# Performance work log

Hardware: AMD Instinct MI355X
Metric: run time of the kernel (lower is better)

Reference implementation:

```python
import jax, jax.numpy as jnp
import numpy as np
import math

D = 1024      # d_model
H = 4096      # expert hidden
E = 8         # num_experts
K = 2         # top_k
CAP_FACTOR = 1.25
B, S = 4, 2048
T = B * S
CAP = int(math.ceil(CAP_FACTOR * T * K / E))  # 2560


def setup_inputs() -> dict:
    key = jax.random.key(0)
    ks = jax.random.split(key, 6)
    x  = jax.random.normal(ks[0], (B, S, D), dtype=jnp.float32)
    Wr = jax.random.normal(ks[1], (D, E), dtype=jnp.float32) * (1.0 / np.sqrt(D))
    W1 = jax.random.normal(ks[2], (E, D, H), dtype=jnp.float32) * (1.0 / np.sqrt(D))
    b1 = jnp.zeros((E, H), dtype=jnp.float32)
    W2 = jax.random.normal(ks[3], (E, H, D), dtype=jnp.float32) * (1.0 / np.sqrt(H))
    b2 = jnp.zeros((E, D), dtype=jnp.float32)
    return {"x": x, "Wr": Wr, "W1": W1, "b1": b1, "W2": W2, "b2": b2}


def reference(x, Wr, W1, b1, W2, b2):
    x_flat = x.reshape(T, D)

    # ---- Router: top-k softmax gating (temp = 1.0), renormalized weights ----
    logits = jnp.einsum('td,de->te', x_flat, Wr)
    probs = jax.nn.softmax(logits, axis=-1)
    topk_w, topk_idx = jax.lax.top_k(probs, K)            # [T,K]
    topk_w = topk_w / jnp.sum(topk_w, axis=-1, keepdims=True)

    # ---- Vectorized capacity-based dispatch ----
    e = topk_idx.reshape(-1)                               # [T*K] expert id per pair
    onehot = jax.nn.one_hot(e, E, dtype=jnp.int32)         # [T*K, E]
    pos_all = jnp.cumsum(onehot, axis=0) - 1               # slot within expert
    pos = jnp.take_along_axis(pos_all, e[:, None], axis=1)[:, 0]
    keep = pos < CAP
    # dropped pairs go to a dummy slot E*CAP (sliced off / zero-padded)
    dest = jnp.where(keep, e * CAP + pos, E * CAP)         # [T*K]

    x_pairs = jnp.repeat(x_flat, K, axis=0)                # [T*K, D]
    buf = jnp.zeros((E * CAP + 1, D), dtype=x.dtype).at[dest].set(x_pairs)
    expert_in = buf[:E * CAP].reshape(E, CAP, D)

    # ---- Grouped expert MLP (GELU) ----
    h = jax.nn.gelu(jnp.einsum('ecd,edh->ech', expert_in, W1) + b1[:, None, :])
    expert_out = jnp.einsum('ech,ehd->ecd', h, W2) + b2[:, None, :]

    # ---- Combine: gather back and weight; dropped tokens get zeros ----
    out_pad = jnp.concatenate(
        [expert_out.reshape(E * CAP, D), jnp.zeros((1, D), dtype=x.dtype)], axis=0)
    y_pairs = out_pad[dest] * topk_w.reshape(-1)[:, None]  # [T*K, D]
    y_flat = y_pairs.reshape(T, K, D).sum(axis=1)
    return y_flat.reshape(B, S, D)
```

## Files before the change

kernel.cpp:

```cpp
#include <hip/hip_runtime.h>
#include <stdint.h>

#define D_MODEL 1024
#define H_DIM   4096
#define NE      8
#define NCAP    2560
#define NTOK    8192
#define NPAIR   (NTOK * 2)

typedef __attribute__((ext_vector_type(8))) __bf16 bf16x8;
typedef __attribute__((ext_vector_type(4))) float  f32x4;
typedef __attribute__((ext_vector_type(8))) unsigned short ushort8;

__device__ __forceinline__ unsigned short f2bf(float f) {
  union { float f; unsigned u; } v; v.f = f;
  unsigned r = v.u + 0x7fffu + ((v.u >> 16) & 1u);
  return (unsigned short)(r >> 16);
}
__device__ __forceinline__ float bf2f(unsigned short s) {
  union { unsigned u; float f; } v; v.u = ((unsigned)s) << 16;
  return v.f;
}
__device__ __forceinline__ float gelu_tanh(float x) {
  float u = 0.7978845608028654f * (x + 0.044715f * x * x * x);
  float e = __expf(2.0f * u);
  float th = 1.0f - 2.0f / (e + 1.0f);
  return 0.5f * x * (1.0f + th);
}
__device__ __forceinline__ void load_lds16(const void* g, void* l) {
  __builtin_amdgcn_global_load_lds(
      (const __attribute__((address_space(1))) unsigned int*)g,
      (__attribute__((address_space(3))) unsigned int*)l, 16, 0, 0);
}

__global__ __launch_bounds__(256) void router_kernel(
    const float* __restrict__ x, const float* __restrict__ Wr,
    int* __restrict__ pair_e, float* __restrict__ pair_w) {
  int lane = threadIdx.x & 63;
  int t = blockIdx.x * 4 + (threadIdx.x >> 6);
  float acc[NE];
#pragma unroll
  for (int e = 0; e < NE; ++e) acc[e] = 0.0f;
  const float* xr = x + (size_t)t * D_MODEL;
  for (int d = lane; d < D_MODEL; d += 64) {
    float xv = xr[d];
#pragma unroll
    for (int e = 0; e < NE; ++e) acc[e] = fmaf(xv, Wr[d * NE + e], acc[e]);
  }
#pragma unroll
  for (int off = 32; off > 0; off >>= 1) {
#pragma unroll
    for (int e = 0; e < NE; ++e) acc[e] += __shfl_down(acc[e], off, 64);
  }
  if (lane == 0) {
    int i1 = 0;
#pragma unroll
    for (int e = 1; e < NE; ++e) if (acc[e] > acc[i1]) i1 = e;
    int i2 = (i1 == 0) ? 1 : 0;
#pragma unroll
    for (int e = 0; e < NE; ++e) if (e != i1 && acc[e] > acc[i2]) i2 = e;
    float p2 = expf(acc[i2] - acc[i1]);
    float inv = 1.0f / (1.0f + p2);
    pair_e[t * 2]     = i1;  pair_e[t * 2 + 1] = i2;
    pair_w[t * 2]     = inv;
    pair_w[t * 2 + 1] = p2 * inv;
  }
}

__global__ void assign_kernel(const int* __restrict__ pair_e,
                              int* __restrict__ pair_dest,
                              int* __restrict__ counts) {
  int lane = threadIdx.x;
  int run[NE];
#pragma unroll
  for (int e = 0; e < NE; ++e) run[e] = 0;
  unsigned long long below = (lane == 63) ? 0x7fffffffffffffffull
                                          : ((1ull << lane) - 1ull);
  for (int base = 0; base < NPAIR; base += 64) {
    int i = base + lane;
    int e = pair_e[i];
    int pos = 0;
#pragma unroll
    for (int ex = 0; ex < NE; ++ex) {
      unsigned long long m = __ballot(e == ex);
      if (e == ex) pos = run[ex] + __popcll(m & below);
      run[ex] += __popcll(m);
    }
    bool keep = pos < NCAP;
    pair_dest[i] = keep ? (e * NCAP + pos) : (NE * NCAP);
  }
  if (lane == 0) {
#pragma unroll
    for (int e = 0; e < NE; ++e) counts[e] = run[e] < NCAP ? run[e] : NCAP;
  }
}

__global__ __launch_bounds__(64) void dispatch_kernel(
    const float* __restrict__ x, const int* __restrict__ pair_dest,
    unsigned short* __restrict__ Xd) {
  int i = blockIdx.x;
  int dest = pair_dest[i];
  if (dest >= NE * NCAP) return;
  int lane = threadIdx.x;
  int t = i >> 1;
  const float4* xr = (const float4*)(x + (size_t)t * D_MODEL);
  ushort4* dr = (ushort4*)(Xd + (size_t)dest * D_MODEL);
#pragma unroll
  for (int c = 0; c < 4; ++c) {
    float4 v = xr[lane + c * 64];
    ushort4 o;
    o.x = f2bf(v.x); o.y = f2bf(v.y); o.z = f2bf(v.z); o.w = f2bf(v.w);
    dr[lane + c * 64] = o;
  }
}

__global__ __launch_bounds__(256) void transpose_cvt(
    const float* __restrict__ src, unsigned short* __restrict__ dst,
    int R, int C) {
  __shared__ float tile[64][65];
  int e = blockIdx.z;
  int c0 = blockIdx.x * 64, r0 = blockIdx.y * 64;
  int col = threadIdx.x & 63, rr = threadIdx.x >> 6;
  const float* s = src + (size_t)e * R * C;
#pragma unroll
  for (int it = 0; it < 16; ++it) {
    int row = it * 4 + rr;
    tile[row][col] = s[(size_t)(r0 + row) * C + c0 + col];
  }
  __syncthreads();
  unsigned short* d = dst + (size_t)e * R * C;
#pragma unroll
  for (int it = 0; it < 16; ++it) {
    int crow = it * 4 + rr;
    d[(size_t)(c0 + crow) * R + r0 + col] = f2bf(tile[col][crow]);
  }
}

__global__ __launch_bounds__(256, 2) void moe_gemm(
    const unsigned short* __restrict__ Abase,
    const unsigned short* __restrict__ Bbase,
    const float* __restrict__ bias,
    unsigned short* __restrict__ Cout,
    const int* __restrict__ counts,
    int M, int N, int K, int NBM, int do_gelu) {
  __shared__ char smem[65536];
  const int e = blockIdx.z;
  int r = blockIdx.x;
  int grp = r >> 4, lid = r & 15;
  int mg = NBM >> 2;
  int gm = grp % mg, gn = grp / mg;
  const int m0 = (gm * 4 + (lid & 3)) * 128;
  const int n0 = (gn * 4 + (lid >> 2)) * 128;
  const int cnt = counts[e];
  if (m0 >= cnt) return;

  const int tid = threadIdx.x;
  const int lane = tid & 63;
  const int wid = tid >> 6;
  const int wm = (wid & 1) * 64;
  const int wn = (wid >> 1) * 64;

  const unsigned short* A = Abase + (size_t)e * M * K;
  const unsigned short* B = Bbase + (size_t)e * N * K;

  f32x4 acc[4][4];
  f32x4 zero = {0.f, 0.f, 0.f, 0.f};
#pragma unroll
  for (int i = 0; i < 4; ++i)
#pragma unroll
    for (int j = 0; j < 4; ++j) acc[i][j] = zero;

  char* As0 = smem;
  char* Bs0 = smem + 16384;
  char* As1 = smem + 32768;
  char* Bs1 = smem + 49152;

  const unsigned short* ga[4];
  const unsigned short* gb[4];
  int ldso[4];
#pragma unroll
  for (int c = 0; c < 4; ++c) {
    int ci = c * 256 + wid * 64 + lane;
    int srow = ci >> 3;
    int sgc = (ci & 7) ^ (srow & 7);
    ga[c] = A + (size_t)(m0 + srow) * K + sgc * 8;
    gb[c] = B + (size_t)(n0 + srow) * K + sgc * 8;
    ldso[c] = (c * 256 + wid * 64) * 16;
  }

  auto stage = [&](char* As, char* Bs) {
#pragma unroll
    for (int c = 0; c < 4; ++c) {
      load_lds16(ga[c], As + ldso[c]);
      ga[c] += 64;
      load_lds16(gb[c], Bs + ldso[c]);
      gb[c] += 64;
    }
  };
  auto compute = [&](char* As, char* Bs) {
#pragma unroll
    for (int kk = 0; kk < 2; ++kk) {
      bf16x8 af[4], bfr[4];
      int lc = kk * 4 + (lane >> 4);
#pragma unroll
      for (int f = 0; f < 4; ++f) {
        int ar = wm + f * 16 + (lane & 15);
        af[f] = *(const bf16x8*)(As + ar * 128 + ((lc ^ (ar & 7)) * 16));
        int br = wn + f * 16 + (lane & 15);
        bfr[f] = *(const bf16x8*)(Bs + br * 128 + ((lc ^ (br & 7)) * 16));
      }
#pragma unroll
      for (int i = 0; i < 4; ++i)
#pragma unroll
        for (int j = 0; j < 4; ++j)
          acc[i][j] = __builtin_amdgcn_mfma_f32_16x16x32_bf16(
              af[i], bfr[j], acc[i][j], 0, 0, 0);
    }
  };

  const int KT = K >> 6;
  stage(As0, Bs0);
  for (int kt = 0; kt < KT; kt += 2) {
    __syncthreads();
    if (kt + 1 < KT) stage(As1, Bs1);
    compute(As0, Bs0);
    __syncthreads();
    if (kt + 2 < KT) stage(As0, Bs0);
    compute(As1, Bs1);
  }

  const float* be = bias + (size_t)e * N;
#pragma unroll
  for (int i = 0; i < 4; ++i) {
    int rbase = wm + i * 16 + (lane >> 4) * 4;
#pragma unroll
    for (int j = 0; j < 4; ++j) {
      int col = wn + j * 16 + (lane & 15);
      float bv = be[n0 + col];
#pragma unroll
      for (int r2 = 0; r2 < 4; ++r2) {
        float xv = acc[i][j][r2] + bv;
        if (do_gelu) xv = gelu_tanh(xv);
        *(unsigned short*)(smem + (rbase + r2) * 256 + col * 2) = f2bf(xv);
      }
    }
  }
  __syncthreads();
  const int r16 = tid >> 4, c16 = tid & 15;
#pragma unroll
  for (int it = 0; it < 8; ++it) {
    int row = it * 16 + r16;
    ushort8 v = *(const ushort8*)(smem + row * 256 + c16 * 16);
    *(ushort8*)(Cout + ((size_t)e * M + m0 + row) * N + n0 + c16 * 8) = v;
  }
}

__global__ __launch_bounds__(256) void combine_kernel(
    const unsigned short* __restrict__ Ebuf,
    const int* __restrict__ pair_dest,
    const float* __restrict__ pair_w,
    float* __restrict__ out) {
  int t = blockIdx.x;
  int d0 = threadIdx.x * 4;
  float4 r = {0.f, 0.f, 0.f, 0.f};
#pragma unroll
  for (int k = 0; k < 2; ++k) {
    int dest = pair_dest[t * 2 + k];
    if (dest < NE * NCAP) {
      float w = pair_w[t * 2 + k];
      ushort4 v = *(const ushort4*)(Ebuf + (size_t)dest * D_MODEL + d0);
      r.x += w * bf2f(v.x); r.y += w * bf2f(v.y);
      r.z += w * bf2f(v.z); r.w += w * bf2f(v.w);
    }
  }
  *(float4*)(out + (size_t)t * D_MODEL + d0) = r;
}

extern "C" void kernel_launch(void* const* d_in, const int* in_sizes, int n_in,
                              void* d_out, int out_size, void* d_ws, size_t ws_size,
                              hipStream_t stream) {
  const float* x  = (const float*)d_in[0];
  const float* Wr = (const float*)d_in[1];
  const float* W1 = (const float*)d_in[2];
  const float* b1 = (const float*)d_in[3];
  const float* W2 = (const float*)d_in[4];
  const float* b2 = (const float*)d_in[5];
  float* out = (float*)d_out;

  char* ws = (char*)d_ws;
  unsigned short* W1T  = (unsigned short*)(ws + 0);
  unsigned short* W2T  = (unsigned short*)(ws + 67108864);
  unsigned short* Xd   = (unsigned short*)(ws + 134217728);
  unsigned short* Ebuf = Xd;
  unsigned short* Hbuf = (unsigned short*)(ws + 176160768);
  int*   pair_e    = (int*)(ws + 343932928);
  float* pair_w    = (float*)(ws + 343998464);
  int*   pair_dest = (int*)(ws + 344064000);
  int*   counts    = (int*)(ws + 344129536);

  transpose_cvt<<<dim3(H_DIM / 64, D_MODEL / 64, NE), 256, 0, stream>>>(W1, W1T, D_MODEL, H_DIM);
  transpose_cvt<<<dim3(D_MODEL / 64, H_DIM / 64, NE), 256, 0, stream>>>(W2, W2T, H_DIM, D_MODEL);

  router_kernel<<<NTOK / 4, 256, 0, stream>>>(x, Wr, pair_e, pair_w);
  assign_kernel<<<1, 64, 0, stream>>>(pair_e, pair_dest, counts);
  dispatch_kernel<<<NPAIR, 64, 0, stream>>>(x, pair_dest, Xd);

  moe_gemm<<<dim3((NCAP / 128) * (H_DIM / 128), 1, NE), 256, 0, stream>>>(
      Xd, W1T, b1, Hbuf, counts, NCAP, H_DIM, D_MODEL, NCAP / 128, 1);
  moe_gemm<<<dim3((NCAP / 128) * (D_MODEL / 128), 1, NE), 256, 0, stream>>>(
      Hbuf, W2T, b2, Ebuf, counts, NCAP, D_MODEL, H_DIM, NCAP / 128, 0);

  combine_kernel<<<NTOK, 256, 0, stream>>>(Ebuf, pair_dest, pair_w, out);
}
```

Before: 890.5 us.

## Parallelize capacity assignment scan and single-buffer GEMM LDS for higher occupancy

The serial single-wave assign kernel is replaced by a 1024-thread block in which each thread counts 16 pairs, followed by wave shuffle prefix sums and a cross-wave scan in LDS. This targets the long serial loop over all pairs. Separately, the expert GEMM drops LDS double buffering to 32KB and raises launch bounds to 4 blocks per CU, relying on occupancy rather than in-block prefetch to hide global-to-LDS latency. This adds two syncs per K step and loses the overlap of loads with compute.

New measurement: 770.1 us. 1.16x faster.

```diff
diff --git a/kernel.cpp b/kernel.cpp
--- a/kernel.cpp
+++ b/kernel.cpp
@@ -67,31 +67,63 @@
   }
 }
 
-__global__ void assign_kernel(const int* __restrict__ pair_e,
-                              int* __restrict__ pair_dest,
-                              int* __restrict__ counts) {
-  int lane = threadIdx.x;
-  int run[NE];
-#pragma unroll
-  for (int e = 0; e < NE; ++e) run[e] = 0;
-  unsigned long long below = (lane == 63) ? 0x7fffffffffffffffull
-                                          : ((1ull << lane) - 1ull);
-  for (int base = 0; base < NPAIR; base += 64) {
-    int i = base + lane;
-    int e = pair_e[i];
-    int pos = 0;
-#pragma unroll
-    for (int ex = 0; ex < NE; ++ex) {
-      unsigned long long m = __ballot(e == ex);
-      if (e == ex) pos = run[ex] + __popcll(m & below);
-      run[ex] += __popcll(m);
-    }
-    bool keep = pos < NCAP;
-    pair_dest[i] = keep ? (e * NCAP + pos) : (NE * NCAP);
-  }
-  if (lane == 0) {
-#pragma unroll
-    for (int e = 0; e < NE; ++e) counts[e] = run[e] < NCAP ? run[e] : NCAP;
+__global__ __launch_bounds__(1024) void assign_kernel(
+    const int* __restrict__ pair_e, int* __restrict__ pair_dest,
+    int* __restrict__ counts) {
+  __shared__ int wtot[16][NE];
+  const int tid = threadIdx.x;
+  const int lane = tid & 63, w = tid >> 6;
+
+  int ids[16];
+  const int4* pe = (const int4*)(pair_e + tid * 16);
+#pragma unroll
+  for (int q = 0; q < 4; ++q) {
+    int4 v = pe[q];
+    ids[q * 4 + 0] = v.x; ids[q * 4 + 1] = v.y;
+    ids[q * 4 + 2] = v.z; ids[q * 4 + 3] = v.w;
+  }
+  int c[NE];
+#pragma unroll
+  for (int e = 0; e < NE; ++e) c[e] = 0;
+#pragma unroll
+  for (int j = 0; j < 16; ++j) c[ids[j]]++;
+
+  int incl[NE];
+#pragma unroll
+  for (int e = 0; e < NE; ++e) incl[e] = c[e];
+#pragma unroll
+  for (int d = 1; d < 64; d <<= 1) {
+#pragma unroll
+    for (int e = 0; e < NE; ++e) {
+      int u = __shfl_up(incl[e], d, 64);
+      if (lane >= d) incl[e] += u;
+    }
+  }
+  if (lane == 63) {
+#pragma unroll
+    for (int e = 0; e < NE; ++e) wtot[w][e] = incl[e];
+  }
+  __syncthreads();
+  if (tid < NE) {
+    int run = 0;
+#pragma unroll
+    for (int ww = 0; ww < 16; ++ww) {
+      int t2 = wtot[ww][tid];
+      wtot[ww][tid] = run;
+      run += t2;
+    }
+    counts[tid] = run < NCAP ? run : NCAP;
+  }
+  __syncthreads();
+
+  int off[NE];
+#pragma unroll
+  for (int e = 0; e < NE; ++e) off[e] = wtot[w][e] + incl[e] - c[e];
+#pragma unroll
+  for (int j = 0; j < 16; ++j) {
+    int e = ids[j];
+    int pos = off[e]++;
+    pair_dest[tid * 16 + j] = (pos < NCAP) ? (e * NCAP + pos) : (NE * NCAP);
   }
 }
 
@@ -136,14 +168,14 @@
   }
 }
 
-__global__ __launch_bounds__(256, 2) void moe_gemm(
+__global__ __launch_bounds__(256, 4) void moe_gemm(
     const unsigned short* __restrict__ Abase,
     const unsigned short* __restrict__ Bbase,
     const float* __restrict__ bias,
     unsigned short* __restrict__ Cout,
     const int* __restrict__ counts,
     int M, int N, int K, int NBM, int do_gelu) {
-  __shared__ char smem[65536];
+  __shared__ char smem[32768];
   const int e = blockIdx.z;
   int r = blockIdx.x;
   int grp = r >> 4, lid = r & 15;
@@ -170,10 +202,8 @@
 #pragma unroll
     for (int j = 0; j < 4; ++j) acc[i][j] = zero;
 
-  char* As0 = smem;
-  char* Bs0 = smem + 16384;
-  char* As1 = smem + 32768;
-  char* Bs1 = smem + 49152;
+  char* As = smem;
+  char* Bs = smem + 16384;
 
   const unsigned short* ga[4];
   const unsigned short* gb[4];
@@ -188,7 +218,8 @@
     ldso[c] = (c * 256 + wid * 64) * 16;
   }
 
-  auto stage = [&](char* As, char* Bs) {
+  const int KT = K >> 6;
+  for (int kt = 0; kt < KT; ++kt) {
 #pragma unroll
     for (int c = 0; c < 4; ++c) {
       load_lds16(ga[c], As + ldso[c]);
@@ -196,8 +227,7 @@
       load_lds16(gb[c], Bs + ldso[c]);
       gb[c] += 64;
     }
-  };
-  auto compute = [&](char* As, char* Bs) {
+    __syncthreads();
 #pragma unroll
     for (int kk = 0; kk < 2; ++kk) {
       bf16x8 af[4], bfr[4];
@@ -216,17 +246,7 @@
           acc[i][j] = __builtin_amdgcn_mfma_f32_16x16x32_bf16(
               af[i], bfr[j], acc[i][j], 0, 0, 0);
     }
-  };
-
-  const int KT = K >> 6;
-  stage(As0, Bs0);
-  for (int kt = 0; kt < KT; kt += 2) {
     __syncthreads();
-    if (kt + 1 < KT) stage(As1, Bs1);
-    compute(As0, Bs0);
-    __syncthreads();
-    if (kt + 2 < KT) stage(As0, Bs0);
-    compute(As1, Bs1);
   }
 
   const float* be = bias + (size_t)e * N;
@@ -302,7 +322,7 @@
   transpose_cvt<<<dim3(D_MODEL / 64, H_DIM / 64, NE), 256, 0, stream>>>(W2, W2T, H_DIM, D_MODEL);
 
   router_kernel<<<NTOK / 4, 256, 0, stream>>>(x, Wr, pair_e, pair_w);
-  assign_kernel<<<1, 64, 0, stream>>>(pair_e, pair_dest, counts);
+  assign_kernel<<<1, 1024, 0, stream>>>(pair_e, pair_dest, counts);
   dispatch_kernel<<<NPAIR, 64, 0, stream>>>(x, pair_dest, Xd);
 
   moe_gemm<<<dim3((NCAP / 128) * (H_DIM / 128), 1, NE), 256, 0, stream>>>(
```
